# Performance work log

Hardware: AMD Instinct MI355X
Metric: run time of the kernel (lower is better)

Reference implementation:

```python
import jax, jax.numpy as jnp
import numpy as np

N_NODES = 50000
N_EDGES = 1600000
D_IN = 256
N_HEADS = 4
D_OUT = 32
NEG_SLOPE = 0.2


def setup_inputs() -> dict:
    key = jax.random.key(0)
    ks = jax.random.split(key, 7)
    return {
        "feat": jax.random.normal(ks[0], (N_NODES, D_IN), dtype=jnp.float32),
        "fc_w": jax.random.normal(ks[1], (N_HEADS * D_OUT, D_IN), dtype=jnp.float32) * 0.05,
        "attn_l": jax.random.normal(ks[2], (1, N_HEADS, D_OUT), dtype=jnp.float32) * 0.1,
        "attn_r": jax.random.normal(ks[3], (1, N_HEADS, D_OUT), dtype=jnp.float32) * 0.1,
        "bias": jax.random.normal(ks[4], (N_HEADS * D_OUT,), dtype=jnp.float32) * 0.01,
        "src": jax.random.randint(ks[5], (N_EDGES,), 0, N_NODES, dtype=jnp.int32),
        "dst": jax.random.randint(ks[6], (N_EDGES,), 0, N_NODES, dtype=jnp.int32),
    }


def reference(feat, fc_w, attn_l, attn_r, bias, src, dst):
    N = feat.shape[0]
    H, D = attn_l.shape[1], attn_l.shape[2]
    # projected features: [N, H, D] (torch Linear: x @ W.T)
    h = (feat @ fc_w.T).reshape(N, H, D)
    # per-node attention logits: [N, H]
    el = (h * attn_l).sum(-1)
    er = (h * attn_r).sum(-1)
    # per-edge score with leaky relu: [E, H]
    e = el[src] + er[dst]
    e = jnp.where(e > 0, e, NEG_SLOPE * e)
    # edge softmax normalized over incoming edges of each dst node
    m = jax.ops.segment_max(e, dst, num_segments=N)
    m = jnp.where(jnp.isfinite(m), m, 0.0)  # nodes with no in-edges
    ex = jnp.exp(e - m[dst])
    denom = jax.ops.segment_sum(ex, dst, num_segments=N)
    a = ex / jnp.maximum(denom[dst], 1e-9)  # [E, H]
    # weighted scatter-aggregate: [N, H, D]
    msg = h[src] * a[:, :, None]
    out = jax.ops.segment_sum(msg, dst, num_segments=N)
    out = out + bias.reshape(1, H, D)
    return out
```

## Files before the change

kernel.cpp:

```cpp
#include <hip/hip_runtime.h>
#include <hip/hip_bf16.h>
#include <math.h>

#define D_IN   256
#define HD     128
#define NHEAD  4
#define NEG_SLOPE 0.2f
#define CHUNK 32
#define MAXB  1024
#define BCAP  2560

typedef _Float16 h8 __attribute__((ext_vector_type(8)));
typedef _Float16 h4 __attribute__((ext_vector_type(4)));
typedef _Float16 h2 __attribute__((ext_vector_type(2)));
typedef float f4 __attribute__((ext_vector_type(4)));

#define SWZ(row, byte) ((byte) ^ (((row) & 7) << 4))

__global__ __launch_bounds__(256) void wconv_k(const float* __restrict__ fcw,
                                               unsigned short* __restrict__ wf16) {
    int i = blockIdx.x * 256 + threadIdx.x;
    float4 v = *(const float4*)&fcw[i * 4];
    h4 p = {(_Float16)v.x, (_Float16)v.y, (_Float16)v.z, (_Float16)v.w};
    *(h4*)&wf16[i * 4] = p;
}

__global__ __launch_bounds__(256) void fused_k(
        const float* __restrict__ feat, const unsigned short* __restrict__ wf16,
        const float* __restrict__ attn_l, const float* __restrict__ attn_r,
        unsigned int* __restrict__ hbuf, float* __restrict__ el, float* __restrict__ er,
        const int* __restrict__ src, const int* __restrict__ dst,
        int* __restrict__ gcur, unsigned int* __restrict__ pairs,
        int N, int E, int B, int GB) {
    __shared__ __align__(16) unsigned char smem[64 * 512];
    const int t = threadIdx.x;

    if ((int)blockIdx.x >= GB) {
        int* lcnt  = (int*)smem;
        int* lbase = lcnt + MAXB;
        for (int i = t; i < B; i += 256) lcnt[i] = 0;
        __syncthreads();
        const int base = ((int)blockIdx.x - GB) * 4096;
        int sv[16], dv[16];
        #pragma unroll
        for (int k = 0; k < 16; ++k) {
            int idx = base + k * 256 + t;
            if (idx < E) {
                sv[k] = src[idx];
                dv[k] = dst[idx];
                atomicAdd(&lcnt[dv[k] >> 6], 1);
            } else dv[k] = -1;
        }
        __syncthreads();
        for (int i = t; i < B; i += 256) {
            int c = lcnt[i];
            lbase[i] = c ? atomicAdd(&gcur[i], c) : 0;
            lcnt[i] = 0;
        }
        __syncthreads();
        #pragma unroll
        for (int k = 0; k < 16; ++k) {
            if (dv[k] >= 0) {
                int b = dv[k] >> 6;
                int r = lbase[b] + atomicAdd(&lcnt[b], 1);
                if (r < BCAP)
                    pairs[(size_t)b * BCAP + r] =
                        ((unsigned int)sv[k] << 6) | (unsigned int)(dv[k] & 63);
            }
        }
        return;
    }

    unsigned char* lds_raw = smem;
    const int l  = t & 63;
    const int w  = t >> 6;
    const int l4 = l >> 4;
    const int lm = l & 15;
    const int n0 = blockIdx.x * 64;

    h8 breg[2][8];
    #pragma unroll
    for (int jt = 0; jt < 2; ++jt) {
        const unsigned short* wrow = wf16 + (size_t)(w * 32 + jt * 16 + lm) * D_IN;
        #pragma unroll
        for (int ks = 0; ks < 8; ++ks)
            breg[jt][ks] = *(const h8*)&wrow[ks * 32 + l4 * 8];
    }

    #pragma unroll
    for (int i = 0; i < 16; ++i) {
        int idx = t + 256 * i;
        int row = idx >> 6, c4 = idx & 63;
        float4 v = make_float4(0.f, 0.f, 0.f, 0.f);
        if (n0 + row < N) v = *(const float4*)&feat[(size_t)(n0 + row) * D_IN + c4 * 4];
        h4 p = {(_Float16)v.x, (_Float16)v.y, (_Float16)v.z, (_Float16)v.w};
        *(h4*)(lds_raw + row * 512 + SWZ(row, c4 * 8)) = p;
    }
    __syncthreads();

    f4 acc[4][2] = {};
    #pragma unroll
    for (int ks = 0; ks < 8; ++ks) {
        #pragma unroll
        for (int mt = 0; mt < 4; ++mt) {
            int row = mt * 16 + lm;
            h8 af = *(const h8*)(lds_raw + row * 512 + SWZ(row, (ks * 32 + l4 * 8) * 2));
            acc[mt][0] = __builtin_amdgcn_mfma_f32_16x16x32_f16(af, breg[0][ks], acc[mt][0], 0, 0, 0);
            acc[mt][1] = __builtin_amdgcn_mfma_f32_16x16x32_f16(af, breg[1][ks], acc[mt][1], 0, 0, 0);
        }
    }

    float al[2], ar[2];
    #pragma unroll
    for (int jt = 0; jt < 2; ++jt) {
        al[jt] = attn_l[w * 32 + jt * 16 + lm];
        ar[jt] = attn_r[w * 32 + jt * 16 + lm];
    }
    #pragma unroll
    for (int mt = 0; mt < 4; ++mt) {
        #pragma unroll
        for (int r = 0; r < 4; ++r) {
            float vl = acc[mt][0][r] * al[0] + acc[mt][1][r] * al[1];
            float vr = acc[mt][0][r] * ar[0] + acc[mt][1][r] * ar[1];
            #pragma unroll
            for (int o = 1; o < 16; o <<= 1) {
                vl += __shfl_xor(vl, o);
                vr += __shfl_xor(vr, o);
            }
            int node = n0 + mt * 16 + l4 * 4 + r;
            if (lm == 0 && node < N) {
                el[node * NHEAD + w] = vl;
                er[node * NHEAD + w] = vr;
            }
        }
    }

    __syncthreads();
    unsigned short* hl = (unsigned short*)lds_raw;
    #pragma unroll
    for (int mt = 0; mt < 4; ++mt)
        #pragma unroll
        for (int jt = 0; jt < 2; ++jt)
            #pragma unroll
            for (int r = 0; r < 4; ++r) {
                int node_local = mt * 16 + l4 * 4 + r;
                int ch = w * 32 + jt * 16 + lm;
                _Float16 hf = (_Float16)acc[mt][jt][r];
                hl[node_local * 128 + ch] = __builtin_bit_cast(unsigned short, hf);
            }
    __syncthreads();
    const unsigned int* hu = (const unsigned int*)lds_raw;
    #pragma unroll
    for (int i = 0; i < 16; ++i) {
        int idx = t + 256 * i;
        int row = idx >> 6, c = idx & 63;
        if (n0 + row < N) hbuf[(size_t)(n0 + row) * 64 + c] = hu[row * 64 + c];
    }
}

__global__ __launch_bounds__(256) void bucket_k(const unsigned int* __restrict__ pairs,
                                                const int* __restrict__ gcur,
                                                int* __restrict__ row_start,
                                                int* __restrict__ degs,
                                                int* __restrict__ srcs, int N) {
    __shared__ int cnt64[64];
    __shared__ int base64[64];
    const int b = blockIdx.x;
    const int t = threadIdx.x;
    const int lo = b * BCAP;
    const int len = min(gcur[b], BCAP);
    if (t < 64) cnt64[t] = 0;
    __syncthreads();
    for (int i = t; i < len; i += 256)
        atomicAdd(&cnt64[pairs[lo + i] & 63], 1);
    __syncthreads();
    if (t < 64) {
        int v = cnt64[t];
        int x = v;
        #pragma unroll
        for (int o = 1; o < 64; o <<= 1) {
            int y = __shfl_up(x, o);
            if (t >= o) x += y;
        }
        int excl = lo + x - v;
        base64[t] = excl;
        int d = b * 64 + t;
        if (d < N) { row_start[d] = excl; degs[d] = v; }
        cnt64[t] = 0;
    }
    __syncthreads();
    for (int i = lo + t; i < lo + len; i += 256) {
        unsigned int p = pairs[i];
        int ld = p & 63;
        int r = atomicAdd(&cnt64[ld], 1);
        srcs[base64[ld] + r] = (int)(p >> 6);
    }
}

__global__ __launch_bounds__(64) void agg_k(
        const int* __restrict__ row_start, const int* __restrict__ degs,
        const int* __restrict__ srcs,
        const float* __restrict__ el, const float* __restrict__ er,
        const unsigned int* __restrict__ hbuf, const float* __restrict__ bias,
        float* __restrict__ out, int N) {
    __shared__ float exw[CHUNK * NHEAD];
    __shared__ int s_lds[CHUNK];
    const int d = blockIdx.x;
    const int l = threadIdx.x;
    const int he = l >> 4, es = l & 15;
    const int half = l >> 5, cl = l & 31;
    const int hc = cl >> 3;
    const int base = row_start[d];
    const int deg  = degs[d];
    const float erd = er[d * NHEAD + he];

    f4 acc = {0.f, 0.f, 0.f, 0.f};
    float den = 0.f;

    for (int c0 = 0; c0 < deg; c0 += CHUNK) {
        const int clen = min(CHUNK, deg - c0);
        __syncthreads();
        int s0 = -1, s1 = -1;
        if (es < clen)      s0 = srcs[base + c0 + es];
        if (es + 16 < clen) s1 = srcs[base + c0 + es + 16];
        float e0 = 0.f, e1 = 0.f;
        if (s0 >= 0) e0 = el[s0 * NHEAD + he];
        if (s1 >= 0) e1 = el[s1 * NHEAD + he];
        if (s0 >= 0) {
            float v = e0 + erd;
            v = v > 0.f ? v : NEG_SLOPE * v;
            float ex = __expf(v);
            if (he == 0) s_lds[es] = s0;
            exw[es * NHEAD + he] = ex;
            den += ex;
        }
        if (s1 >= 0) {
            float v = e1 + erd;
            v = v > 0.f ? v : NEG_SLOPE * v;
            float ex = __expf(v);
            if (he == 0) s_lds[es + 16] = s1;
            exw[(es + 16) * NHEAD + he] = ex;
            den += ex;
        }
        __syncthreads();
        for (int jj = 0; jj < clen; jj += 8) {
            uint2 hv[4];
            float ex4[4];
            int e2v[4];
            #pragma unroll
            for (int k = 0; k < 4; ++k) {
                int e2 = jj + 2 * k + half;
                e2v[k] = (e2 < clen) ? e2 : -1;
                if (e2v[k] >= 0) {
                    int s = s_lds[e2];
                    hv[k] = *(const uint2*)&hbuf[(size_t)s * 64 + cl * 2];
                    ex4[k] = exw[e2 * NHEAD + hc];
                }
            }
            #pragma unroll
            for (int k = 0; k < 4; ++k) {
                if (e2v[k] >= 0) {
                    h2 p0 = __builtin_bit_cast(h2, hv[k].x);
                    h2 p1 = __builtin_bit_cast(h2, hv[k].y);
                    acc[0] += (float)p0[0] * ex4[k];
                    acc[1] += (float)p0[1] * ex4[k];
                    acc[2] += (float)p1[0] * ex4[k];
                    acc[3] += (float)p1[1] * ex4[k];
                }
            }
        }
    }

    #pragma unroll
    for (int k = 0; k < 4; ++k) acc[k] += __shfl_xor(acc[k], 32);
    #pragma unroll
    for (int o = 1; o < 16; o <<= 1) den += __shfl_xor(den, o);
    float denc = __shfl(den, hc << 4);
    float r = 1.0f / fmaxf(denc, 1e-9f);

    if (half == 0) {
        float4 b4 = *(const float4*)&bias[cl * 4];
        float4 o4 = make_float4(acc[0] * r + b4.x, acc[1] * r + b4.y,
                                acc[2] * r + b4.z, acc[3] * r + b4.w);
        *(float4*)&out[(size_t)d * HD + cl * 4] = o4;
    }
}

extern "C" void kernel_launch(void* const* d_in, const int* in_sizes, int n_in,
                              void* d_out, int out_size, void* d_ws, size_t ws_size,
                              hipStream_t stream) {
    const float* feat   = (const float*)d_in[0];
    const float* fcw    = (const float*)d_in[1];
    const float* attn_l = (const float*)d_in[2];
    const float* attn_r = (const float*)d_in[3];
    const float* bias   = (const float*)d_in[4];
    const int*   src    = (const int*)d_in[5];
    const int*   dst    = (const int*)d_in[6];
    float* out = (float*)d_out;

    const int N = in_sizes[0] / D_IN;
    const int E = in_sizes[5];
    const int B = (N + 63) >> 6;

    unsigned int* hbuf = (unsigned int*)d_ws;
    float* el        = (float*)(hbuf + (size_t)N * 64);
    float* er        = el + (size_t)N * NHEAD;
    unsigned short* wf16 = (unsigned short*)(er + (size_t)N * NHEAD);
    unsigned int* pairs = (unsigned int*)(wf16 + HD * D_IN);
    int*   srcs      = (int*)(pairs + (size_t)B * BCAP);
    int*   row_start = srcs + (size_t)B * BCAP;
    int*   degs      = row_start + N;
    int*   gcur      = degs + N;

    const int GB  = (N + 63) / 64;
    const int ebl = (E + 4095) / 4096;

    hipMemsetAsync(gcur, 0, (size_t)B * sizeof(int), stream);
    wconv_k<<<(HD * D_IN / 4 + 255) / 256, 256, 0, stream>>>(fcw, wf16);
    fused_k<<<GB + ebl, 256, 0, stream>>>(feat, wf16, attn_l, attn_r, hbuf, el, er,
                                          src, dst, gcur, pairs, N, E, B, GB);
    bucket_k<<<B, 256, 0, stream>>>(pairs, gcur, row_start, degs, srcs, N);
    agg_k<<<N, 64, 0, stream>>>(row_start, degs, srcs, el, er, hbuf, bias, out, N);
}
```

Before: 122.2 us.

## Fold attention vectors into projection weights and pack two dst nodes per agg block

```diff
diff --git a/kernel.cpp b/kernel.cpp
--- a/kernel.cpp
+++ b/kernel.cpp
@@ -18,21 +18,39 @@
 #define SWZ(row, byte) ((byte) ^ (((row) & 7) << 4))
 
 __global__ __launch_bounds__(256) void wconv_k(const float* __restrict__ fcw,
-                                               unsigned short* __restrict__ wf16) {
-    int i = blockIdx.x * 256 + threadIdx.x;
-    float4 v = *(const float4*)&fcw[i * 4];
-    h4 p = {(_Float16)v.x, (_Float16)v.y, (_Float16)v.z, (_Float16)v.w};
-    *(h4*)&wf16[i * 4] = p;
+                                               const float* __restrict__ attn_l,
+                                               const float* __restrict__ attn_r,
+                                               unsigned short* __restrict__ wf16,
+                                               unsigned short* __restrict__ wlr) {
+    const int t = threadIdx.x;
+    if (blockIdx.x < 32) {
+        int i = blockIdx.x * 256 + t;
+        float4 v = *(const float4*)&fcw[i * 4];
+        h4 p = {(_Float16)v.x, (_Float16)v.y, (_Float16)v.z, (_Float16)v.w};
+        *(h4*)&wf16[i * 4] = p;
+        return;
+    }
+    for (int j = 0; j < 8; ++j) {
+        const float* av = (j < 4) ? &attn_l[j * 32] : &attn_r[(j - 4) * 32];
+        const int wr = (j & 3) * 32;
+        float s = 0.f;
+        #pragma unroll 8
+        for (int dd = 0; dd < 32; ++dd)
+            s += av[dd] * fcw[(size_t)(wr + dd) * D_IN + t];
+        _Float16 hf = (_Float16)s;
+        wlr[j * D_IN + t] = __builtin_bit_cast(unsigned short, hf);
+        wlr[(j + 8) * D_IN + t] = 0;
+    }
 }
 
 __global__ __launch_bounds__(256) void fused_k(
         const float* __restrict__ feat, const unsigned short* __restrict__ wf16,
-        const float* __restrict__ attn_l, const float* __restrict__ attn_r,
+        const unsigned short* __restrict__ wlr,
         unsigned int* __restrict__ hbuf, float* __restrict__ el, float* __restrict__ er,
         const int* __restrict__ src, const int* __restrict__ dst,
         int* __restrict__ gcur, unsigned int* __restrict__ pairs,
         int N, int E, int B, int GB) {
-    __shared__ __align__(16) unsigned char smem[64 * 512];
+    __shared__ __align__(16) unsigned char smem[32 * 512];
     const int t = threadIdx.x;
 
     if ((int)blockIdx.x >= GB) {
@@ -76,19 +94,10 @@
     const int w  = t >> 6;
     const int l4 = l >> 4;
     const int lm = l & 15;
-    const int n0 = blockIdx.x * 64;
-
-    h8 breg[2][8];
-    #pragma unroll
-    for (int jt = 0; jt < 2; ++jt) {
-        const unsigned short* wrow = wf16 + (size_t)(w * 32 + jt * 16 + lm) * D_IN;
-        #pragma unroll
-        for (int ks = 0; ks < 8; ++ks)
-            breg[jt][ks] = *(const h8*)&wrow[ks * 32 + l4 * 8];
-    }
-
-    #pragma unroll
-    for (int i = 0; i < 16; ++i) {
+    const int n0 = blockIdx.x * 32;
+
+    #pragma unroll
+    for (int i = 0; i < 8; ++i) {
         int idx = t + 256 * i;
         int row = idx >> 6, c4 = idx & 63;
         float4 v = make_float4(0.f, 0.f, 0.f, 0.f);
@@ -98,39 +107,38 @@
     }
     __syncthreads();
 
-    f4 acc[4][2] = {};
+    const unsigned short* w0 = wf16 + (size_t)(w * 32 + lm) * D_IN;
+    const unsigned short* w1 = wf16 + (size_t)(w * 32 + 16 + lm) * D_IN;
+    const unsigned short* we = wlr + (size_t)lm * D_IN;
+
+    f4 a00 = {}, a01 = {}, a10 = {}, a11 = {}, ae0 = {}, ae1 = {};
     #pragma unroll
     for (int ks = 0; ks < 8; ++ks) {
-        #pragma unroll
-        for (int mt = 0; mt < 4; ++mt) {
-            int row = mt * 16 + lm;
-            h8 af = *(const h8*)(lds_raw + row * 512 + SWZ(row, (ks * 32 + l4 * 8) * 2));
-            acc[mt][0] = __builtin_amdgcn_mfma_f32_16x16x32_f16(af, breg[0][ks], acc[mt][0], 0, 0, 0);
-            acc[mt][1] = __builtin_amdgcn_mfma_f32_16x16x32_f16(af, breg[1][ks], acc[mt][1], 0, 0, 0);
-        }
-    }
-
-    float al[2], ar[2];
-    #pragma unroll
-    for (int jt = 0; jt < 2; ++jt) {
-        al[jt] = attn_l[w * 32 + jt * 16 + lm];
-        ar[jt] = attn_r[w * 32 + jt * 16 + lm];
-    }
-    #pragma unroll
-    for (int mt = 0; mt < 4; ++mt) {
-        #pragma unroll
-        for (int r = 0; r < 4; ++r) {
-            float vl = acc[mt][0][r] * al[0] + acc[mt][1][r] * al[1];
-            float vr = acc[mt][0][r] * ar[0] + acc[mt][1][r] * ar[1];
+        const int ko = ks * 32 + l4 * 8;
+        h8 b0 = *(const h8*)&w0[ko];
+        h8 b1 = *(const h8*)&w1[ko];
+        h8 be = *(const h8*)&we[ko];
+        h8 af0 = *(const h8*)(lds_raw + lm * 512 + SWZ(lm, ko * 2));
+        h8 af1 = *(const h8*)(lds_raw + (16 + lm) * 512 + SWZ(16 + lm, ko * 2));
+        a00 = __builtin_amdgcn_mfma_f32_16x16x32_f16(af0, b0, a00, 0, 0, 0);
+        a01 = __builtin_amdgcn_mfma_f32_16x16x32_f16(af0, b1, a01, 0, 0, 0);
+        ae0 = __builtin_amdgcn_mfma_f32_16x16x32_f16(af0, be, ae0, 0, 0, 0);
+        a10 = __builtin_amdgcn_mfma_f32_16x16x32_f16(af1, b0, a10, 0, 0, 0);
+        a11 = __builtin_amdgcn_mfma_f32_16x16x32_f16(af1, b1, a11, 0, 0, 0);
+        ae1 = __builtin_amdgcn_mfma_f32_16x16x32_f16(af1, be, ae1, 0, 0, 0);
+    }
+
+    if (lm < 8) {
+        #pragma unroll
+        for (int mt = 0; mt < 2; ++mt) {
+            f4 ae = mt ? ae1 : ae0;
             #pragma unroll
-            for (int o = 1; o < 16; o <<= 1) {
-                vl += __shfl_xor(vl, o);
-                vr += __shfl_xor(vr, o);
-            }
-            int node = n0 + mt * 16 + l4 * 4 + r;
-            if (lm == 0 && node < N) {
-                el[node * NHEAD + w] = vl;
-                er[node * NHEAD + w] = vr;
+            for (int r = 0; r < 4; ++r) {
+                int node = n0 + mt * 16 + l4 * 4 + r;
+                if (node < N) {
+                    if (lm < 4) el[node * NHEAD + lm] = ae[r];
+                    else        er[node * NHEAD + (lm - 4)] = ae[r];
+                }
             }
         }
     }
@@ -138,20 +146,23 @@
     __syncthreads();
     unsigned short* hl = (unsigned short*)lds_raw;
     #pragma unroll
-    for (int mt = 0; mt < 4; ++mt)
-        #pragma unroll
-        for (int jt = 0; jt < 2; ++jt)
+    for (int mt = 0; mt < 2; ++mt) {
+        #pragma unroll
+        for (int jt = 0; jt < 2; ++jt) {
+            f4 av = mt ? (jt ? a11 : a10) : (jt ? a01 : a00);
             #pragma unroll
             for (int r = 0; r < 4; ++r) {
                 int node_local = mt * 16 + l4 * 4 + r;
                 int ch = w * 32 + jt * 16 + lm;
-                _Float16 hf = (_Float16)acc[mt][jt][r];
+                _Float16 hf = (_Float16)av[r];
                 hl[node_local * 128 + ch] = __builtin_bit_cast(unsigned short, hf);
             }
+        }
+    }
     __syncthreads();
     const unsigned int* hu = (const unsigned int*)lds_raw;
     #pragma unroll
-    for (int i = 0; i < 16; ++i) {
+    for (int i = 0; i < 8; ++i) {
         int idx = t + 256 * i;
         int row = idx >> 6, c = idx & 63;
         if (n0 + row < N) hbuf[(size_t)(n0 + row) * 64 + c] = hu[row * 64 + c];
@@ -197,16 +208,20 @@
     }
 }
 
-__global__ __launch_bounds__(64) void agg_k(
+__global__ __launch_bounds__(128) void agg_k(
         const int* __restrict__ row_start, const int* __restrict__ degs,
         const int* __restrict__ srcs,
         const float* __restrict__ el, const float* __restrict__ er,
         const unsigned int* __restrict__ hbuf, const float* __restrict__ bias,
         float* __restrict__ out, int N) {
-    __shared__ float exw[CHUNK * NHEAD];
-    __shared__ int s_lds[CHUNK];
-    const int d = blockIdx.x;
-    const int l = threadIdx.x;
+    __shared__ float exw[2][CHUNK * NHEAD];
+    __shared__ int s_lds[2][CHUNK];
+    const int wv = threadIdx.x >> 6;
+    const int l  = threadIdx.x & 63;
+    const int d  = blockIdx.x * 2 + wv;
+    if (d >= N) return;
+    float* exb = exw[wv];
+    int*   slb = s_lds[wv];
     const int he = l >> 4, es = l & 15;
     const int half = l >> 5, cl = l & 31;
     const int hc = cl >> 3;
@@ -219,7 +234,6 @@
 
     for (int c0 = 0; c0 < deg; c0 += CHUNK) {
         const int clen = min(CHUNK, deg - c0);
-        __syncthreads();
         int s0 = -1, s1 = -1;
         if (es < clen)      s0 = srcs[base + c0 + es];
         if (es + 16 < clen) s1 = srcs[base + c0 + es + 16];
@@ -230,19 +244,18 @@
             float v = e0 + erd;
             v = v > 0.f ? v : NEG_SLOPE * v;
             float ex = __expf(v);
-            if (he == 0) s_lds[es] = s0;
-            exw[es * NHEAD + he] = ex;
+            if (he == 0) slb[es] = s0;
+            exb[es * NHEAD + he] = ex;
             den += ex;
         }
         if (s1 >= 0) {
             float v = e1 + erd;
             v = v > 0.f ? v : NEG_SLOPE * v;
             float ex = __expf(v);
-            if (he == 0) s_lds[es + 16] = s1;
-            exw[(es + 16) * NHEAD + he] = ex;
+            if (he == 0) slb[es + 16] = s1;
+            exb[(es + 16) * NHEAD + he] = ex;
             den += ex;
         }
-        __syncthreads();
         for (int jj = 0; jj < clen; jj += 8) {
             uint2 hv[4];
             float ex4[4];
@@ -252,9 +265,9 @@
                 int e2 = jj + 2 * k + half;
                 e2v[k] = (e2 < clen) ? e2 : -1;
                 if (e2v[k] >= 0) {
-                    int s = s_lds[e2];
+                    int s = slb[e2];
                     hv[k] = *(const uint2*)&hbuf[(size_t)s * 64 + cl * 2];
-                    ex4[k] = exw[e2 * NHEAD + hc];
+                    ex4[k] = exb[e2 * NHEAD + hc];
                 }
             }
             #pragma unroll
@@ -306,19 +319,20 @@
     float* el        = (float*)(hbuf + (size_t)N * 64);
     float* er        = el + (size_t)N * NHEAD;
     unsigned short* wf16 = (unsigned short*)(er + (size_t)N * NHEAD);
-    unsigned int* pairs = (unsigned int*)(wf16 + HD * D_IN);
+    unsigned short* wlr  = wf16 + HD * D_IN;
+    unsigned int* pairs = (unsigned int*)(wlr + 16 * D_IN);
     int*   srcs      = (int*)(pairs + (size_t)B * BCAP);
     int*   row_start = srcs + (size_t)B * BCAP;
     int*   degs      = row_start + N;
     int*   gcur      = degs + N;
 
-    const int GB  = (N + 63) / 64;
+    const int GB  = (N + 31) / 32;
     const int ebl = (E + 4095) / 4096;
 
     hipMemsetAsync(gcur, 0, (size_t)B * sizeof(int), stream);
-    wconv_k<<<(HD * D_IN / 4 + 255) / 256, 256, 0, stream>>>(fcw, wf16);
-    fused_k<<<GB + ebl, 256, 0, stream>>>(feat, wf16, attn_l, attn_r, hbuf, el, er,
+    wconv_k<<<33, 256, 0, stream>>>(fcw, attn_l, attn_r, wf16, wlr);
+    fused_k<<<GB + ebl, 256, 0, stream>>>(feat, wf16, wlr, hbuf, el, er,
                                           src, dst, gcur, pairs, N, E, B, GB);
     bucket_k<<<B, 256, 0, stream>>>(pairs, gcur, row_start, degs, srcs, N);
-    agg_k<<<N, 64, 0, stream>>>(row_start, degs, srcs, el, er, hbuf, bias, out, N);
-}
+    agg_k<<<(N + 1) / 2, 128, 0, stream>>>(row_start, degs, srcs, el, er, hbuf, bias, out, N);
+}
```

Result: slower. 152.0 us (+24.4%).
